# Optimization experiments

Hardware: AMD Instinct MI355X
Metric: run time of the kernel (lower is better)

Reference implementation:

```python
import jax, jax.numpy as jnp
import numpy as np

EMBED_DIM = 1024
NUM_HEADS = 16
HEAD_DIM = EMBED_DIM // NUM_HEADS
B, N = 4, 2048
EPS = 1e-5


def rotate_half(x):
    x2d = x.reshape(x.shape[:-1] + (-1, 2))
    x1, x2 = x2d[..., 0], x2d[..., 1]
    return jnp.stack([-x2, x1], axis=-1).reshape(x.shape)


def apply_rotary_emb(freqs, t):
    return t * freqs[0] + rotate_half(t) * freqs[1]


def setup_inputs() -> dict:
    key = jax.random.key(0)
    ks = jax.random.split(key, 12)
    d = EMBED_DIM
    inp = {
        "x": jax.random.normal(ks[0], (B, N, d), jnp.float32),
        "encoding": jax.random.normal(ks[1], (2, N, HEAD_DIM), jnp.float32),
        "Wqkv_w": jax.random.normal(ks[2], (d, 3 * d), jnp.float32) * (1.0 / np.sqrt(d)),
        "Wqkv_b": jnp.zeros((3 * d,), jnp.float32),
        "out_w": jax.random.normal(ks[3], (d, d), jnp.float32) * (1.0 / np.sqrt(d)),
        "out_b": jnp.zeros((d,), jnp.float32),
        "ffn0_w": jax.random.normal(ks[4], (2 * d, 2 * d), jnp.float32) * (1.0 / np.sqrt(2 * d)),
        "ffn0_b": jnp.zeros((2 * d,), jnp.float32),
        "ln_scale": jnp.ones((2 * d,), jnp.float32),
        "ln_bias": jnp.zeros((2 * d,), jnp.float32),
        "ffn3_w": jax.random.normal(ks[5], (2 * d, d), jnp.float32) * (1.0 / np.sqrt(2 * d)),
        "ffn3_b": jnp.zeros((d,), jnp.float32),
    }
    return inp


def reference(x, encoding, Wqkv_w, Wqkv_b, out_w, out_b, ffn0_w, ffn0_b, ln_scale, ln_bias, ffn3_w, ffn3_b):
    b, n, d = x.shape
    # fused QKV projection
    qkv = jnp.einsum('bnd,de->bne', x, Wqkv_w) + Wqkv_b
    qkv = qkv.reshape(b, n, NUM_HEADS, HEAD_DIM, 3).transpose(0, 2, 1, 3, 4)  # (b,h,n,hd,3)
    q, k, v = qkv[..., 0], qkv[..., 1], qkv[..., 2]
    # RoPE (encoding broadcasts over batch/heads)
    q = apply_rotary_emb(encoding, q)
    k = apply_rotary_emb(encoding, k)
    # attention (no mask)
    scale = 1.0 / jnp.sqrt(jnp.asarray(HEAD_DIM, x.dtype))
    logits = jnp.einsum('bhqd,bhkd->bhqk', q, k) * scale
    attn = jax.nn.softmax(logits, axis=-1)
    context = jnp.einsum('bhqk,bhkd->bhqd', attn, v)
    message = context.transpose(0, 2, 1, 3).reshape(b, n, d)
    message = jnp.einsum('bnd,de->bne', message, out_w) + out_b
    # FFN: concat -> Dense -> LayerNorm -> GELU(exact) -> Dense
    h = jnp.concatenate([x, message], axis=-1)
    h = jnp.einsum('bnd,de->bne', h, ffn0_w) + ffn0_b
    mu = jnp.mean(h, axis=-1, keepdims=True)
    var = jnp.mean(jnp.square(h - mu), axis=-1, keepdims=True)
    h = (h - mu) * jax.lax.rsqrt(var + EPS) * ln_scale + ln_bias
    h = jax.nn.gelu(h, approximate=False)
    res = jnp.einsum('bnd,de->bne', h, ffn3_w) + ffn3_b
    return x + res
```

## Files before the change

### kernel.cpp

```cpp
#include <hip/hip_runtime.h>
#include <hip/hip_bf16.h>
#include <math.h>

typedef __bf16 bf16x8 __attribute__((ext_vector_type(8)));
typedef float f32x4 __attribute__((ext_vector_type(4)));

#define MFMA16(a, b, c) __builtin_amdgcn_mfma_f32_16x16x32_bf16((a), (b), (c), 0, 0, 0)

__device__ __forceinline__ void gload16(const void* g, void* l) {
  __builtin_amdgcn_global_load_lds((const __attribute__((address_space(1))) void*)g,
                                   (__attribute__((address_space(3))) void*)l, 16, 0, 0);
}

#define BARRIER asm volatile("s_barrier" ::: "memory")

__device__ __forceinline__ void tr_body(float (*tile)[33], const float* __restrict__ in,
                                        int ldin, __bf16* __restrict__ out, int ldo,
                                        int n0, int k0, int t) {
  int tx = t & 31, ty = t >> 5;
#pragma unroll
  for (int r = 0; r < 32; r += 8)
    tile[ty + r][tx] = in[(size_t)(k0 + ty + r) * ldin + n0 + tx];
  __syncthreads();
#pragma unroll
  for (int r = 0; r < 32; r += 8)
    out[(size_t)(n0 + ty + r) * ldo + k0 + tx] = (__bf16)tile[tx][ty + r];
}

__global__ __launch_bounds__(256) void prep1(
    const float* __restrict__ wqkv, __bf16* __restrict__ wT_qkv,
    const float* __restrict__ wffn0, __bf16* __restrict__ wT_ffn0,
    __bf16* __restrict__ w0bT,
    const float* __restrict__ wffn3, __bf16* __restrict__ wT_ffn3,
    const float* __restrict__ wout, __bf16* __restrict__ wout_bf,
    const float* __restrict__ bqkv, float* __restrict__ bqkv_p,
    const float* __restrict__ bout, float* __restrict__ bias_part,
    const float* __restrict__ x, __bf16* __restrict__ h_in,
    const float* __restrict__ enc, float* __restrict__ encT) {
  __shared__ float tile[32][33];
  const int bid = blockIdx.x;
  const int t = threadIdx.x;

  if (bid < 3072) {
    int bx = bid % 96, by = bid / 96;
    int n0 = bx * 32, k0 = by * 32;
    int tx = t & 31, ty = t >> 5;
#pragma unroll
    for (int r = 0; r < 32; r += 8)
      tile[ty + r][tx] = wqkv[(size_t)(k0 + ty + r) * 3072 + n0 + tx];
    __syncthreads();
#pragma unroll
    for (int r = 0; r < 32; r += 8) {
      int n = n0 + ty + r;
      int h = n / 192, rem = n % 192, hd = rem / 3, which = rem % 3;
      int np = which * 1024 + h * 64 + hd;
      wT_qkv[(size_t)np * 1024 + k0 + tx] = (__bf16)tile[tx][ty + r];
    }
  } else if (bid < 5120) {
    int lb = bid - 3072, bx = lb % 64, by = lb / 64;
    tr_body(tile, wffn0, 2048, wT_ffn0, 2048, bx * 32, by * 32, t);
  } else if (bid < 7168) {
    int lb = bid - 5120, bx = lb % 64, by = lb / 64;
    tr_body(tile, wffn0 + (size_t)1024 * 2048, 2048, w0bT, 1024, bx * 32, by * 32, t);
  } else if (bid < 9216) {
    int lb = bid - 7168, bx = lb % 32, by = lb / 32;
    tr_body(tile, wffn3, 1024, wT_ffn3, 2048, bx * 32, by * 32, t);
  } else if (bid < 9728) {
    int id = (bid - 9216) * 256 + t;
    const float* src = wout + (size_t)id * 8;
    __bf16 tmp[8];
#pragma unroll
    for (int e = 0; e < 8; ++e) tmp[e] = (__bf16)src[e];
    *(uint4*)(wout_bf + (size_t)id * 8) = *(uint4*)tmp;
  } else if (bid < 9740) {
    int n = (bid - 9728) * 256 + t;
    if (n < 3072) {
      int h = n / 192, rem = n % 192, hd = rem / 3, which = rem % 3;
      bqkv_p[which * 1024 + h * 64 + hd] = bqkv[n];
    }
  } else if (bid < 9868) {
    int lb = bid - 9740;
    int n = (lb % 8) * 256 + t;
    int e0 = (lb / 8) * 64;
    float s = 0.f;
#pragma unroll 4
    for (int e = 0; e < 64; ++e)
      s += bout[e0 + e] * wffn0[(size_t)(1024 + e0 + e) * 2048 + n];
    bias_part[(size_t)(lb / 8) * 2048 + n] = s;
  } else if (bid < 13964) {
    int id = (bid - 9868) * 256 + t;
    int row = id >> 7, cc = id & 127;
    const float* src = x + (size_t)row * 1024 + cc * 8;
    __bf16 tmp[8];
#pragma unroll
    for (int e = 0; e < 8; ++e) tmp[e] = (__bf16)src[e];
    *(uint4*)(h_in + (size_t)row * 2048 + cc * 8) = *(uint4*)tmp;
  } else {
    int lb = bid - 13964;
    int tab = lb >> 7, lb2 = lb & 127;
    int n0 = (lb2 & 1) * 32;
    int k0 = (lb2 >> 1) * 32;
    int tx = t & 31, ty = t >> 5;
#pragma unroll
    for (int r = 0; r < 32; r += 8)
      tile[ty + r][tx] = enc[(size_t)tab * 131072 + (size_t)(k0 + ty + r) * 64 + n0 + tx];
    __syncthreads();
#pragma unroll
    for (int r = 0; r < 32; r += 8)
      encT[(size_t)tab * 131072 + (size_t)(n0 + ty + r) * 2048 + k0 + tx] = tile[tx][ty + r];
  }
}

__global__ __launch_bounds__(256) void prep2(
    const __bf16* __restrict__ w0bT, const __bf16* __restrict__ wout_bf,
    __bf16* __restrict__ wT_ffn0,
    const float* __restrict__ bias_part, const float* __restrict__ bffn0,
    float* __restrict__ bffn0_f) {
  const int bid = blockIdx.x;
  const int t = threadIdx.x;
  if (bid >= 128) {
    int n = (bid - 128) * 256 + t;
    float s = bffn0[n];
#pragma unroll
    for (int y = 0; y < 16; ++y) s += bias_part[(size_t)y * 2048 + n];
    bffn0_f[n] = s;
    return;
  }
  __shared__ __attribute__((aligned(16))) __bf16 As[128 * 64];
  __shared__ __attribute__((aligned(16))) __bf16 Bs[128 * 64];
  const int row0A = (bid % 16) * 128;
  const int row0B = (bid / 16) * 128;
  const int wave = t >> 6, lane = t & 63;
  const int wm = wave >> 1, wn = wave & 1;
  const int g = lane >> 4, lr = lane & 15;
  f32x4 acc[4][4] = {};
  for (int k0 = 0; k0 < 1024; k0 += 64) {
#pragma unroll
    for (int p = 0; p < 4; ++p) {
      int cbase = (wave * 4 + p) * 64;
      int ci = cbase + lane;
      int r = ci >> 3, cp = ci & 7, cl = cp ^ (r & 7);
      gload16(w0bT + (size_t)(row0A + r) * 1024 + k0 + cl * 8, &As[cbase * 8]);
      gload16(wout_bf + (size_t)(row0B + r) * 1024 + k0 + cl * 8, &Bs[cbase * 8]);
    }
    __syncthreads();
#pragma unroll
    for (int kk = 0; kk < 2; ++kk) {
      bf16x8 af[4], bfr[4];
#pragma unroll
      for (int mt = 0; mt < 4; ++mt) {
        int r = wm * 64 + mt * 16 + lr, c = kk * 4 + g;
        af[mt] = *(const bf16x8*)((char*)As + r * 128 + ((c ^ (r & 7)) * 16));
      }
#pragma unroll
      for (int nt = 0; nt < 4; ++nt) {
        int r = wn * 64 + nt * 16 + lr, c = kk * 4 + g;
        bfr[nt] = *(const bf16x8*)((char*)Bs + r * 128 + ((c ^ (r & 7)) * 16));
      }
#pragma unroll
      for (int mt = 0; mt < 4; ++mt)
#pragma unroll
        for (int nt = 0; nt < 4; ++nt)
          acc[mt][nt] = MFMA16(af[mt], bfr[nt], acc[mt][nt]);
    }
    __syncthreads();
  }
#pragma unroll
  for (int mt = 0; mt < 4; ++mt) {
    int grow_base = row0A + wm * 64 + mt * 16 + g * 4;
#pragma unroll
    for (int nt = 0; nt < 4; ++nt) {
      int gcol = row0B + wn * 64 + nt * 16 + lr;
#pragma unroll
      for (int j = 0; j < 4; ++j)
        wT_ffn0[(size_t)(grow_base + j) * 2048 + 1024 + gcol] = (__bf16)acc[mt][nt][j];
    }
  }
}

template <typename OutT, bool HAS_RES, bool HAS_BIAS>
__global__ __launch_bounds__(256) void gemm_kernel(
    const __bf16* __restrict__ A, int lda,
    const __bf16* __restrict__ Bt,
    const float* __restrict__ bias,
    OutT* __restrict__ C, int ldc,
    const float* __restrict__ res,
    int M, int Nn, int K) {
  __shared__ __attribute__((aligned(16))) __bf16 As[128 * 64];
  __shared__ __attribute__((aligned(16))) __bf16 Bs[128 * 64];

  const int t = threadIdx.x;
  const int row0A = blockIdx.x * 128;
  const int row0B = blockIdx.y * 128;
  const int wave = t >> 6, lane = t & 63;
  const int wm = wave >> 1, wn = wave & 1;
  const int g = lane >> 4, lr = lane & 15;

  f32x4 acc[4][4] = {};

  for (int k0 = 0; k0 < K; k0 += 64) {
#pragma unroll
    for (int p = 0; p < 4; ++p) {
      int cbase = (wave * 4 + p) * 64;
      int ci = cbase + lane;
      int r = ci >> 3, cp = ci & 7, cl = cp ^ (r & 7);
      gload16(A + (size_t)(row0A + r) * lda + k0 + cl * 8, &As[cbase * 8]);
      gload16(Bt + (size_t)(row0B + r) * K + k0 + cl * 8, &Bs[cbase * 8]);
    }
    __syncthreads();
#pragma unroll
    for (int kk = 0; kk < 2; ++kk) {
      bf16x8 af[4], bfr[4];
#pragma unroll
      for (int mt = 0; mt < 4; ++mt) {
        int r = wm * 64 + mt * 16 + lr, c = kk * 4 + g;
        af[mt] = *(const bf16x8*)((char*)As + r * 128 + ((c ^ (r & 7)) * 16));
      }
#pragma unroll
      for (int nt = 0; nt < 4; ++nt) {
        int r = wn * 64 + nt * 16 + lr, c = kk * 4 + g;
        bfr[nt] = *(const bf16x8*)((char*)Bs + r * 128 + ((c ^ (r & 7)) * 16));
      }
#pragma unroll
      for (int mt = 0; mt < 4; ++mt)
#pragma unroll
        for (int nt = 0; nt < 4; ++nt)
          acc[mt][nt] = MFMA16(af[mt], bfr[nt], acc[mt][nt]);
    }
    __syncthreads();
  }

  float bias_v[4];
#pragma unroll
  for (int nt = 0; nt < 4; ++nt)
    bias_v[nt] = HAS_BIAS ? bias[row0B + wn * 64 + nt * 16 + lr] : 0.f;
#pragma unroll
  for (int mt = 0; mt < 4; ++mt) {
    int grow_base = row0A + wm * 64 + mt * 16 + g * 4;
#pragma unroll
    for (int nt = 0; nt < 4; ++nt) {
      int gcol = row0B + wn * 64 + nt * 16 + lr;
#pragma unroll
      for (int j = 0; j < 4; ++j) {
        int grow = grow_base + j;
        float v = acc[mt][nt][j] + bias_v[nt];
        if (HAS_RES) v += res[(size_t)grow * ldc + gcol];
        C[(size_t)grow * ldc + gcol] = (OutT)v;
      }
    }
  }
}

template <typename OutT, int MODE>
__global__ __launch_bounds__(512, 2) void gemm256p(
    const __bf16* __restrict__ A, int lda,
    const __bf16* __restrict__ Bt, int ldb,
    const float* __restrict__ bias,
    OutT* __restrict__ C, int ldc, int K,
    __bf16* __restrict__ qb, __bf16* __restrict__ kb,
    __bf16* __restrict__ vtb, const float* __restrict__ encT) {
  __shared__ __attribute__((aligned(16))) __bf16 As[2][256 * 64];
  __shared__ __attribute__((aligned(16))) __bf16 Bs[2][256 * 64];

  const int t = threadIdx.x;
  const int wave = t >> 6, lane = t & 63;
  const int wm = wave >> 2, wn = wave & 3;
  const int g = lane >> 4, lr = lane & 15;
  const int row0A = blockIdx.x * 256, row0B = blockIdx.y * 256;
  const int L = K >> 6;

  f32x4 acc[8][4] = {};

#define STG_A(tile, i)                                                        \
  {                                                                           \
    int cb = ((i) * 8 + wave) * 64;                                           \
    int ci = cb + lane;                                                       \
    int r = ci >> 3, cl = (ci & 7) ^ (r & 7);                                 \
    gload16(A + (size_t)(row0A + r) * lda + (size_t)(tile) * 64 + cl * 8,     \
            &As[(tile) & 1][cb * 8]);                                         \
  }
#define STG_B(tile, i)                                                        \
  {                                                                           \
    int cb = ((i) * 8 + wave) * 64;                                           \
    int ci = cb + lane;                                                       \
    int r = ci >> 3, cl = (ci & 7) ^ (r & 7);                                 \
    gload16(Bt + (size_t)(row0B + r) * ldb + (size_t)(tile) * 64 + cl * 8,    \
            &Bs[(tile) & 1][cb * 8]);                                         \
  }
#define AFRAG(d, mi, ks)                                                      \
  (*(const bf16x8*)((const char*)As[d] + (wm * 128 + (mi) * 16 + lr) * 128 +  \
                    ((((ks) * 4 + g) ^ (lr & 7)) * 16)))
#define BFRAG(d, ni, ks)                                                      \
  (*(const bf16x8*)((const char*)Bs[d] + (wn * 64 + (ni) * 16 + lr) * 128 +   \
                    ((((ks) * 4 + g) ^ (lr & 7)) * 16)))

#pragma unroll
  for (int i = 0; i < 4; ++i) STG_A(0, i);
#pragma unroll
  for (int i = 0; i < 4; ++i) STG_B(0, i);
  STG_A(1, 0);
  STG_A(1, 1);
  asm volatile("s_waitcnt vmcnt(2)" ::: "memory");
  BARRIER;

  for (int tt = 0; tt < L; ++tt) {
    const int d = tt & 1;
    const bool s1 = (tt + 1) < L, s2 = (tt + 2) < L;
    bf16x8 aL[4][2], aH[4][2], bL[2][2], bH[2][2];

#pragma unroll
    for (int mi = 0; mi < 4; ++mi) {
      aL[mi][0] = AFRAG(d, mi, 0);
      aL[mi][1] = AFRAG(d, mi, 1);
    }
#pragma unroll
    for (int ni = 0; ni < 2; ++ni) {
      bL[ni][0] = BFRAG(d, ni, 0);
      bL[ni][1] = BFRAG(d, ni, 1);
    }
    if (s1) { STG_A(tt + 1, 2); STG_A(tt + 1, 3); }
    BARRIER;
    __builtin_amdgcn_s_setprio(1);
#pragma unroll
    for (int mi = 0; mi < 4; ++mi)
#pragma unroll
      for (int ni = 0; ni < 2; ++ni) {
        acc[mi][ni] = MFMA16(aL[mi][0], bL[ni][0], acc[mi][ni]);
        acc[mi][ni] = MFMA16(aL[mi][1], bL[ni][1], acc[mi][ni]);
      }
    __builtin_amdgcn_s_setprio(0);
    BARRIER;

#pragma unroll
    for (int ni = 0; ni < 2; ++ni) {
      bH[ni][0] = BFRAG(d, ni + 2, 0);
      bH[ni][1] = BFRAG(d, ni + 2, 1);
    }
    if (s1) { STG_B(tt + 1, 0); STG_B(tt + 1, 1); }
    BARRIER;
    __builtin_amdgcn_s_setprio(1);
#pragma unroll
    for (int mi = 0; mi < 4; ++mi)
#pragma unroll
      for (int ni = 0; ni < 2; ++ni) {
        acc[mi][ni + 2] = MFMA16(aL[mi][0], bH[ni][0], acc[mi][ni + 2]);
        acc[mi][ni + 2] = MFMA16(aL[mi][1], bH[ni][1], acc[mi][ni + 2]);
      }
    __builtin_amdgcn_s_setprio(0);
    BARRIER;

#pragma unroll
    for (int mi = 0; mi < 4; ++mi) {
      aH[mi][0] = AFRAG(d, mi + 4, 0);
      aH[mi][1] = AFRAG(d, mi + 4, 1);
    }
    if (s1) { STG_B(tt + 1, 2); STG_B(tt + 1, 3); }
    BARRIER;
    __builtin_amdgcn_s_setprio(1);
#pragma unroll
    for (int mi = 0; mi < 4; ++mi)
#pragma unroll
      for (int ni = 0; ni < 2; ++ni) {
        acc[mi + 4][ni + 2] = MFMA16(aH[mi][0], bH[ni][0], acc[mi + 4][ni + 2]);
        acc[mi + 4][ni + 2] = MFMA16(aH[mi][1], bH[ni][1], acc[mi + 4][ni + 2]);
      }
    __builtin_amdgcn_s_setprio(0);
    BARRIER;

    if (s2) { STG_A(tt + 2, 0); STG_A(tt + 2, 1); }
    __builtin_amdgcn_s_setprio(1);
#pragma unroll
    for (int mi = 0; mi < 4; ++mi)
#pragma unroll
      for (int ni = 0; ni < 2; ++ni) {
        acc[mi + 4][ni] = MFMA16(aH[mi][0], bL[ni][0], acc[mi + 4][ni]);
        acc[mi + 4][ni] = MFMA16(aH[mi][1], bL[ni][1], acc[mi + 4][ni]);
      }
    __builtin_amdgcn_s_setprio(0);
    if (s2)
      asm volatile("s_waitcnt vmcnt(2)" ::: "memory");
    else
      asm volatile("s_waitcnt vmcnt(0)" ::: "memory");
    BARRIER;
  }
#undef STG_A
#undef STG_B
#undef AFRAG
#undef BFRAG

  float bias_v[4];
#pragma unroll
  for (int ni = 0; ni < 4; ++ni) bias_v[ni] = bias[row0B + wn * 64 + ni * 16 + lr];

  if (MODE == 0) {
#pragma unroll
    for (int mi = 0; mi < 8; ++mi) {
      int grow_base = row0A + wm * 128 + mi * 16 + g * 4;
#pragma unroll
      for (int ni = 0; ni < 4; ++ni) {
        int gcol = row0B + wn * 64 + ni * 16 + lr;
#pragma unroll
        for (int j = 0; j < 4; ++j)
          C[(size_t)(grow_base + j) * ldc + gcol] = (OutT)(acc[mi][ni][j] + bias_v[ni]);
      }
    }
  } else {
    const int which = blockIdx.y >> 2;
    const int h = (blockIdx.y & 3) * 4 + wn;
    const int b = blockIdx.x >> 3;
    const int bh = b * 16 + h;
    const int ntop = (blockIdx.x & 7) * 256 + wm * 128;

    if (which < 2) {
      __bf16* dst = (which == 0) ? qb : kb;
      const float sc = (which == 0) ? 0.125f * 1.44269504088896f : 1.f;
      const float sgn = (lane & 1) ? 1.f : -1.f;
#pragma unroll
      for (int mi = 0; mi < 8; ++mi) {
#pragma unroll
        for (int ni = 0; ni < 4; ++ni) {
          int hd = ni * 16 + lr;
          const float* p0 = encT + (size_t)hd * 2048 + ntop + mi * 16 + g * 4;
          float4 f0 = *(const float4*)p0;
          float4 f1 = *(const float4*)(p0 + 131072);
#pragma unroll
          for (int j = 0; j < 4; ++j) {
            float v = acc[mi][ni][j] + bias_v[ni];
            float p = __shfl_xor(v, 1, 64);
            float e0 = ((const float*)&f0)[j], e1 = ((const float*)&f1)[j];
            float r = (v * e0 + sgn * p * e1) * sc;
            dst[((size_t)bh * 2048 + ntop + mi * 16 + g * 4 + j) * 64 + hd] = (__bf16)r;
          }
        }
      }
    } else {
      char* lbuf = (char*)As;
      const int wb2 = wave * 16384;
#pragma unroll
      for (int mi = 0; mi < 8; ++mi)
#pragma unroll
        for (int ni = 0; ni < 4; ++ni) {
          int hd = ni * 16 + lr;
          int tok = mi * 16 + g * 4;
          __bf16 w4[4];
#pragma unroll
          for (int j = 0; j < 4; ++j) w4[j] = (__bf16)(acc[mi][ni][j] + bias_v[ni]);
          int ab = wb2 + hd * 256 + ((tok * 2) ^ ((hd & 15) << 4));
          *(uint2*)(lbuf + ab) = *(uint2*)w4;
        }
      __syncthreads();
#pragma unroll
      for (int it = 0; it < 16; ++it) {
        int hd = (lane >> 3) + (it & 7) * 8;
        int slot = (lane & 7) + (it >> 3) * 8;
        int grp = slot >> 3, c = slot & 7;
        int kv0 = grp * 64 + (c >> 2) * 32 + (c & 3) * 4;
        int a1 = wb2 + hd * 256 + ((kv0 * 2) ^ ((hd & 15) << 4));
        int a2 = wb2 + hd * 256 + (((kv0 + 16) * 2) ^ ((hd & 15) << 4));
        uint2 lo = *(uint2*)(lbuf + a1);
        uint2 hi = *(uint2*)(lbuf + a2);
        uint4 o4 = make_uint4(lo.x, lo.y, hi.x, hi.y);
        *(uint4*)(vtb + ((size_t)bh * 64 + hd) * 2048 + ntop + grp * 64 + c * 8) = o4;
      }
    }
  }
}

__global__ __launch_bounds__(256) void attn_kernel(
    const __bf16* __restrict__ q, const __bf16* __restrict__ k,
    const __bf16* __restrict__ vt, __bf16* __restrict__ ctx) {
  __shared__ __attribute__((aligned(16))) __bf16 Ks[2][64 * 64];
  __shared__ __attribute__((aligned(16))) __bf16 Vs[2][64 * 64];

  int nwg = gridDim.x * gridDim.y;
  int bid0 = blockIdx.y * gridDim.x + blockIdx.x;
  int bid = (bid0 & 7) * (nwg >> 3) + (bid0 >> 3);
  const int bh = bid >> 4, qblk = bid & 15;
  const int b = bh >> 4, h = bh & 15;
  const int q0 = qblk * 128;
  const int t = threadIdx.x, wave = t >> 6, lane = t & 63;
  const int g = lane >> 4, lr = lane & 15;
  const int qrow0 = q0 + wave * 32;

  const __bf16* kbase = k + (size_t)bh * 2048 * 64;
  const __bf16* vbase = vt + (size_t)bh * 64 * 2048;

  bf16x8 qf[2][2];
#pragma unroll
  for (int u = 0; u < 2; ++u)
#pragma unroll
    for (int kc = 0; kc < 2; ++kc)
      qf[u][kc] = *(const bf16x8*)(q + ((size_t)bh * 2048 + qrow0 + u * 16 + lr) * 64 +
                                   kc * 32 + g * 8);

  bf16x8 ones;
#pragma unroll
  for (int e = 0; e < 8; ++e) ones[e] = (__bf16)1.0f;

  f32x4 o[2][4] = {};
  f32x4 lacc[2] = {};

#define STAGE_ATTN(buf, kv0)                                                    \
  {                                                                             \
    _Pragma("unroll") for (int p = 0; p < 2; ++p) {                             \
      int cbase = wave * 128 + p * 64;                                          \
      int ci = cbase + lane;                                                    \
      int r = ci >> 3, cp = ci & 7, cl = cp ^ (r & 7);                          \
      gload16(kbase + (size_t)((kv0) + r) * 64 + cl * 8, &Ks[buf][cbase * 8]);  \
      gload16(vbase + (size_t)r * 2048 + (kv0) + cl * 8, &Vs[buf][cbase * 8]);  \
    }                                                                           \
  }

  STAGE_ATTN(0, 0);
  __syncthreads();
  int buf = 0;

  for (int kv0 = 0; kv0 < 2048; kv0 += 64) {
    if (kv0 + 64 < 2048) STAGE_ATTN(buf ^ 1, kv0 + 64);

    f32x4 s[2][4];
    __builtin_amdgcn_s_setprio(1);
#pragma unroll
    for (int nt = 0; nt < 4; ++nt) {
      int r = nt * 16 + lr;
      bf16x8 kf0 = *(const bf16x8*)((char*)Ks[buf] + r * 128 + ((g ^ (r & 7)) * 16));
      bf16x8 kf1 = *(const bf16x8*)((char*)Ks[buf] + r * 128 + (((4 + g) ^ (r & 7)) * 16));
#pragma unroll
      for (int u = 0; u < 2; ++u) {
        f32x4 a = {};
        a = MFMA16(kf0, qf[u][0], a);
        a = MFMA16(kf1, qf[u][1], a);
        s[u][nt] = a;
      }
    }
    __builtin_amdgcn_s_setprio(0);

#pragma unroll
    for (int t2 = 0; t2 < 2; ++t2) {
      bf16x8 pf[2];
#pragma unroll
      for (int u = 0; u < 2; ++u) {
#pragma unroll
        for (int e = 0; e < 8; ++e)
          pf[u][e] = (__bf16)__builtin_amdgcn_exp2f(s[u][2 * t2 + (e >> 2)][e & 3]);
        lacc[u] = MFMA16(ones, pf[u], lacc[u]);
      }
      __builtin_amdgcn_s_setprio(1);
#pragma unroll
      for (int nt = 0; nt < 4; ++nt) {
        int r = nt * 16 + lr;
        bf16x8 vf = *(const bf16x8*)((char*)Vs[buf] + r * 128 + (((t2 * 4 + g) ^ (r & 7)) * 16));
#pragma unroll
        for (int u = 0; u < 2; ++u) o[u][nt] = MFMA16(vf, pf[u], o[u][nt]);
      }
      __builtin_amdgcn_s_setprio(0);
    }
    __syncthreads();
    buf ^= 1;
  }

#pragma unroll
  for (int u = 0; u < 2; ++u) {
    float inv = 1.f / lacc[u][0];
    size_t obase = ((size_t)(b * 2048 + qrow0 + u * 16 + lr)) * 2048 + 1024 + h * 64;
#pragma unroll
    for (int nt = 0; nt < 4; ++nt) {
      __bf16 w4[4];
#pragma unroll
      for (int j = 0; j < 4; ++j) w4[j] = (__bf16)(o[u][nt][j] * inv);
      *(uint2*)(ctx + obase + nt * 16 + g * 4) = *(uint2*)w4;
    }
  }
#undef STAGE_ATTN
}

__global__ __launch_bounds__(256) void ln_gelu(const __bf16* __restrict__ hin,
                                               const float* __restrict__ lns,
                                               const float* __restrict__ lnb,
                                               __bf16* __restrict__ hout) {
  int row = blockIdx.x;
  const __bf16* rp = hin + (size_t)row * 2048;
  int t = threadIdx.x;
  __bf16 tmp[8];
  *(uint4*)tmp = *(const uint4*)(rp + t * 8);
  float vals[8], s = 0.f, s2 = 0.f;
#pragma unroll
  for (int e = 0; e < 8; ++e) {
    float x = (float)tmp[e];
    vals[e] = x;
    s += x;
    s2 += x * x;
  }
#pragma unroll
  for (int m = 1; m < 64; m <<= 1) {
    s += __shfl_xor(s, m, 64);
    s2 += __shfl_xor(s2, m, 64);
  }
  __shared__ float red[8];
  int wave = t >> 6, lane = t & 63;
  if (lane == 0) { red[wave] = s; red[4 + wave] = s2; }
  __syncthreads();
  s = red[0] + red[1] + red[2] + red[3];
  s2 = red[4] + red[5] + red[6] + red[7];
  float mu = s * (1.f / 2048.f);
  float var = s2 * (1.f / 2048.f) - mu * mu;
  float rstd = rsqrtf(var + 1e-5f);
  __bf16 outv[8];
#pragma unroll
  for (int e = 0; e < 8; ++e) {
    int c = t * 8 + e;
    float xh = (vals[e] - mu) * rstd * lns[c] + lnb[c];
    float gg = 0.5f * xh * (1.f + erff(xh * 0.70710678118f));
    outv[e] = (__bf16)gg;
  }
  *(uint4*)(hout + (size_t)row * 2048 + t * 8) = *(uint4*)outv;
}

extern "C" void kernel_launch(void* const* d_in, const int* in_sizes, int n_in,
                              void* d_out, int out_size, void* d_ws, size_t ws_size,
                              hipStream_t stream) {
  const float* x = (const float*)d_in[0];
  const float* enc = (const float*)d_in[1];
  const float* wqkv = (const float*)d_in[2];
  const float* bqkv = (const float*)d_in[3];
  const float* wout = (const float*)d_in[4];
  const float* bout = (const float*)d_in[5];
  const float* wffn0 = (const float*)d_in[6];
  const float* bffn0 = (const float*)d_in[7];
  const float* lns = (const float*)d_in[8];
  const float* lnb = (const float*)d_in[9];
  const float* wffn3 = (const float*)d_in[10];
  const float* bffn3 = (const float*)d_in[11];
  float* out = (float*)d_out;
  char* ws = (char*)d_ws;

  __bf16* wT_qkv = (__bf16*)(ws + 0);
  __bf16* wT_ffn0 = (__bf16*)(ws + 6291456);
  __bf16* wT_ffn3 = (__bf16*)(ws + 14680064);
  __bf16* wout_bf = (__bf16*)(ws + 18874368);
  __bf16* w0bT = (__bf16*)(ws + 20971520);
  float* bias_part = (float*)(ws + 25165824);
  float* bqkv_p = (float*)(ws + 25296896);
  float* bffn0_f = (float*)(ws + 25309184);
  __bf16* h_in = (__bf16*)(ws + 25317376);
  __bf16* ffn0o = (__bf16*)(ws + 58871808);
  __bf16* qb = (__bf16*)(ws + 109203456);
  __bf16* h2 = qb;
  __bf16* kb = (__bf16*)(ws + 125980672);
  __bf16* vtb = (__bf16*)(ws + 142757888);
  float* encT = (float*)(ws + 159535104);

  dim3 blk(256);
  prep1<<<14220, blk, 0, stream>>>(wqkv, wT_qkv, wffn0, wT_ffn0, w0bT, wffn3, wT_ffn3,
                                   wout, wout_bf, bqkv, bqkv_p, bout, bias_part, x, h_in,
                                   enc, encT);
  prep2<<<136, blk, 0, stream>>>(w0bT, wout_bf, wT_ffn0, bias_part, bffn0, bffn0_f);

  gemm256p<__bf16, 1><<<dim3(32, 12), dim3(512), 0, stream>>>(
      h_in, 2048, wT_qkv, 1024, bqkv_p, (__bf16*)nullptr, 0, 1024, qb, kb, vtb, encT);

  attn_kernel<<<dim3(16, 64), blk, 0, stream>>>(qb, kb, vtb, h_in);

  gemm256p<__bf16, 0><<<dim3(32, 8), dim3(512), 0, stream>>>(
      h_in, 2048, wT_ffn0, 2048, bffn0_f, ffn0o, 2048, 2048,
      nullptr, nullptr, nullptr, nullptr);

  ln_gelu<<<8192, blk, 0, stream>>>(ffn0o, lns, lnb, h2);

  gemm_kernel<float, true, true><<<dim3(64, 8), blk, 0, stream>>>(
      h2, 2048, wT_ffn3, bffn3, out, 1024, x, 8192, 1024, 2048);
}
```

Baseline: 365.0 us.

## Vectorize Q/K epilogue stores with interleaved Q layout and LDS-staged K

The QKV GEMM epilogue previously wrote Q and K with scattered scalar bf16 stores. Q is now stored in a token-quad-interleaved layout so each lane writes 8 bytes at once, and the attention kernel's Q fragment load is rewritten to gather from that layout. K is staged through swizzled LDS and written out as coalesced 16-byte rows. This cuts uncoalesced global stores in the projection kernel, at the cost of strided scalar Q loads in attention and an extra LDS round trip and barrier for K.

Measured after the change: 364.1 us (median of 2 runs). No clear change (-0.2%).

```diff
diff --git a/kernel.cpp b/kernel.cpp
--- a/kernel.cpp
+++ b/kernel.cpp
@@ -411,27 +411,60 @@
     const int bh = b * 16 + h;
     const int ntop = (blockIdx.x & 7) * 256 + wm * 128;
 
-    if (which < 2) {
-      __bf16* dst = (which == 0) ? qb : kb;
-      const float sc = (which == 0) ? 0.125f * 1.44269504088896f : 1.f;
+    if (which == 0) {
+      const float sc = 0.125f * 1.44269504088896f;
       const float sgn = (lane & 1) ? 1.f : -1.f;
+      const size_t qbase = (size_t)bh * 131072;
 #pragma unroll
       for (int mi = 0; mi < 8; ++mi) {
+        int tb0 = ((ntop + mi * 16) >> 2) + g;
 #pragma unroll
         for (int ni = 0; ni < 4; ++ni) {
           int hd = ni * 16 + lr;
           const float* p0 = encT + (size_t)hd * 2048 + ntop + mi * 16 + g * 4;
           float4 f0 = *(const float4*)p0;
           float4 f1 = *(const float4*)(p0 + 131072);
+          __bf16 w4[4];
 #pragma unroll
           for (int j = 0; j < 4; ++j) {
             float v = acc[mi][ni][j] + bias_v[ni];
             float p = __shfl_xor(v, 1, 64);
             float e0 = ((const float*)&f0)[j], e1 = ((const float*)&f1)[j];
-            float r = (v * e0 + sgn * p * e1) * sc;
-            dst[((size_t)bh * 2048 + ntop + mi * 16 + g * 4 + j) * 64 + hd] = (__bf16)r;
+            w4[j] = (__bf16)((v * e0 + sgn * p * e1) * sc);
+          }
+          *(uint2*)(qb + qbase + (size_t)tb0 * 256 + hd * 4) = *(uint2*)w4;
+        }
+      }
+    } else if (which == 1) {
+      char* lbuf = (char*)As;
+      const int wb = wave * 16384;
+      const float sgn = (lane & 1) ? 1.f : -1.f;
+#pragma unroll
+      for (int mi = 0; mi < 8; ++mi) {
+#pragma unroll
+        for (int ni = 0; ni < 4; ++ni) {
+          int hd = ni * 16 + lr;
+          const float* p0 = encT + (size_t)hd * 2048 + ntop + mi * 16 + g * 4;
+          float4 f0 = *(const float4*)p0;
+          float4 f1 = *(const float4*)(p0 + 131072);
+#pragma unroll
+          for (int j = 0; j < 4; ++j) {
+            float v = acc[mi][ni][j] + bias_v[ni];
+            float p = __shfl_xor(v, 1, 64);
+            float e0 = ((const float*)&f0)[j], e1 = ((const float*)&f1)[j];
+            __bf16 r = (__bf16)(v * e0 + sgn * p * e1);
+            int ltok = mi * 16 + g * 4 + j;
+            *(__bf16*)(lbuf + wb + ltok * 128 + ((hd * 2) ^ ((ltok & 7) << 4))) = r;
           }
         }
+      }
+      __syncthreads();
+#pragma unroll
+      for (int it = 0; it < 16; ++it) {
+        int ltok = (lane >> 3) + (it & 7) * 8 + (it >> 3) * 64;
+        int o = lane & 7;
+        uint4 val = *(uint4*)(lbuf + wb + ltok * 128 + ((o ^ (ltok & 7)) << 4));
+        *(uint4*)(kb + ((size_t)bh * 2048 + ntop + ltok) * 64 + o * 8) = val;
       }
     } else {
       char* lbuf = (char*)As;
@@ -487,11 +520,17 @@
 
   bf16x8 qf[2][2];
 #pragma unroll
-  for (int u = 0; u < 2; ++u)
-#pragma unroll
-    for (int kc = 0; kc < 2; ++kc)
-      qf[u][kc] = *(const bf16x8*)(q + ((size_t)bh * 2048 + qrow0 + u * 16 + lr) * 64 +
-                                   kc * 32 + g * 8);
+  for (int u = 0; u < 2; ++u) {
+    int tok = qrow0 + u * 16 + lr;
+    const __bf16* qp = q + (size_t)bh * 131072 + (size_t)(tok >> 2) * 256 + (tok & 3);
+#pragma unroll
+    for (int kc = 0; kc < 2; ++kc) {
+      bf16x8 v;
+#pragma unroll
+      for (int e = 0; e < 8; ++e) v[e] = qp[(kc * 32 + g * 8 + e) * 4];
+      qf[u][kc] = v;
+    }
+  }
 
   bf16x8 ones;
 #pragma unroll
```
